# Kernel tuning notes

Hardware: AMD Instinct MI355X
Metric: run time of the kernel (lower is better)

The kernel has to match this reference:

```python
import jax, jax.numpy as jnp
import numpy as np

B, T, H, NH, HD = 2, 2048, 2048, 16, 128


def setup_inputs() -> dict:
    key = jax.random.key(0)
    k1, k2, k3 = jax.random.split(key, 3)
    hidden_states = jax.random.normal(k1, (B, T, H), dtype=jnp.float32)
    w_qkv = jax.random.normal(k2, (3 * H, H), dtype=jnp.float32) * (1.0 / np.sqrt(H))
    w_out = jax.random.normal(k3, (H, H), dtype=jnp.float32) * (1.0 / np.sqrt(H))
    return {"hidden_states": hidden_states, "w_qkv": w_qkv, "w_out": w_out}


def reference(hidden_states, w_qkv, w_out):
    scale = 1.0 / np.sqrt(HD)
    # qkv projection: torch Linear is x @ W.T with W [out, in]
    qkv = jnp.einsum('bth,oh->bto', hidden_states, w_qkv)  # [B, T, 3H]
    q, k, v = jnp.split(qkv, 3, axis=2)
    # [B, NH, T, HD]
    q = q.reshape(B, T, NH, HD).transpose(0, 2, 1, 3)
    k = k.reshape(B, T, NH, HD).transpose(0, 2, 1, 3)
    v = v.reshape(B, T, NH, HD).transpose(0, 2, 1, 3)
    scores = jnp.einsum('bhqd,bhkd->bhqk', q, k) * scale  # [B, NH, T, T]
    mask = jnp.tril(jnp.ones((T, T), dtype=bool))  # causal
    scores = jnp.where(mask[None, None], scores, -jnp.inf)
    probs = jax.nn.softmax(scores, axis=-1)
    attn = jnp.einsum('bhqk,bhkd->bhqd', probs, v)  # [B, NH, T, HD]
    attn = attn.transpose(0, 2, 1, 3).reshape(B, T, H)
    out = jnp.einsum('bth,oh->bto', attn, w_out)
    return out
```

## Files before the change

kernel.cpp:

```cpp
#include <hip/hip_runtime.h>
#include <cstdint>
#include <cstddef>

typedef _Float16 f16x8 __attribute__((ext_vector_type(8)));
typedef _Float16 f16x4 __attribute__((ext_vector_type(4)));
typedef float    f32x4 __attribute__((ext_vector_type(4)));
typedef unsigned short ushort_t;

#define LOG2E 1.4426950408889634f

constexpr int BATCH = 2;
constexpr int TSEQ  = 2048;
constexpr int HID   = 2048;
constexpr int NH    = 16;
constexpr int HD    = 128;
constexpr int GK    = 2048;
constexpr int NKT   = GK / 64;

__device__ inline f32x4 mfma16(f16x8 a, f16x8 b, f32x4 c) {
    return __builtin_amdgcn_mfma_f32_16x16x32_f16(a, b, c, 0, 0, 0);
}

__device__ inline void async_copy16(const void* src, void* dst_lds) {
    __builtin_amdgcn_global_load_lds(
        (const __attribute__((address_space(1))) uint32_t*)src,
        (__attribute__((address_space(3))) uint32_t*)dst_lds, 16, 0, 0);
}

__global__ __launch_bounds__(256)
void cast_f32_f16(const float4* __restrict__ in, f16x4* __restrict__ out, int n4) {
    int i = blockIdx.x * 256 + threadIdx.x;
    if (i >= n4) return;
    float4 v = in[i];
    f16x4 o = { (_Float16)v.x, (_Float16)v.y, (_Float16)v.z, (_Float16)v.w };
    out[i] = o;
}

template <int MODE>
__global__ __launch_bounds__(512, 2)
void gemm_bt(const _Float16* __restrict__ A, const _Float16* __restrict__ B,
             float* __restrict__ C, _Float16* __restrict__ Qo,
             _Float16* __restrict__ Ko, _Float16* __restrict__ Vo, int NB) {
    __shared__ __align__(16) _Float16 As[3][256 * 64];
    __shared__ __align__(16) _Float16 Bs[3][128 * 64];

    const int tid  = threadIdx.x;
    const int lane = tid & 63;
    const int w    = tid >> 6;
    const int l15  = lane & 15;
    const int lq   = lane >> 4;
    const int wr   = w >> 1, wc = w & 1;

    const int bid = (int)blockIdx.x;
    const int cpx = (int)gridDim.x >> 3;
    const int swz = (bid & 7) * cpx + (bid >> 3);
    const int bn  = swz % NB, bm = swz / NB;
    const int m0  = bm * 256, n0 = bn * 128;

    const _Float16* Ab = A + (size_t)m0 * GK;
    const _Float16* Bb = B + (size_t)n0 * GK;

    auto stage = [&](int t, int b) {
        const int k0 = t * 64;
        #pragma unroll
        for (int it = 0; it < 4; ++it) {
            const int slot = it * 512 + tid;
            const int row = slot >> 3, c16 = slot & 7;
            const int srcb = c16 ^ (row & 7);
            async_copy16(Ab + (size_t)row * GK + k0 + srcb * 8,
                         (char*)As[b] + slot * 16);
        }
        #pragma unroll
        for (int it = 0; it < 2; ++it) {
            const int slot = it * 512 + tid;
            const int row = slot >> 3, c16 = slot & 7;
            const int srcb = c16 ^ (row & 7);
            async_copy16(Bb + (size_t)row * GK + k0 + srcb * 8,
                         (char*)Bs[b] + slot * 16);
        }
    };

    f32x4 acc[4][4] = {};

    stage(0, 0);
    stage(1, 1);

    for (int t = 0; t < NKT; ++t) {
        if (t + 1 < NKT) asm volatile("s_waitcnt vmcnt(6)" ::: "memory");
        else             asm volatile("s_waitcnt vmcnt(0)" ::: "memory");
        __builtin_amdgcn_s_barrier();
        __builtin_amdgcn_sched_barrier(0);

        const char* At_ = (const char*)As[t % 3];
        const char* Bt_ = (const char*)Bs[t % 3];

        f16x8 af[4][2], bff[4][2];
        #pragma unroll
        for (int i = 0; i < 4; ++i)
            #pragma unroll
            for (int kk = 0; kk < 2; ++kk) {
                const int ra = wr * 64 + i * 16 + l15;
                af[i][kk]  = *(const f16x8*)(At_ + ra * 128 + (((kk * 4 + lq) ^ (ra & 7)) << 4));
                const int rb = wc * 64 + i * 16 + l15;
                bff[i][kk] = *(const f16x8*)(Bt_ + rb * 128 + (((kk * 4 + lq) ^ (rb & 7)) << 4));
            }

        if (t + 2 < NKT) stage(t + 2, (t + 2) % 3);

        __builtin_amdgcn_s_setprio(1);
        #pragma unroll
        for (int kk = 0; kk < 2; ++kk)
            #pragma unroll
            for (int i = 0; i < 4; ++i)
                #pragma unroll
                for (int j = 0; j < 4; ++j)
                    acc[i][j] = mfma16(af[i][kk], bff[j][kk], acc[i][j]);
        __builtin_amdgcn_s_setprio(0);
    }

    if (MODE == 0) {
        #pragma unroll
        for (int j = 0; j < 4; ++j) {
            const int ncol = n0 + wc * 64 + j * 16 + l15;
            const int which = ncol >> 11;
            const int oo = ncol & 2047;
            const int head = oo >> 7;
            const int d = oo & 127;
            _Float16* dst = (which == 0) ? Qo : (which == 1) ? Ko : Vo;
            const float scl = (which == 0) ? 0.08838834764831845f : 1.0f;
            #pragma unroll
            for (int i = 0; i < 4; ++i) {
                #pragma unroll
                for (int r = 0; r < 4; ++r) {
                    const int m = m0 + wr * 64 + i * 16 + lq * 4 + r;
                    const int b = m >> 11, tt = m & 2047;
                    dst[((size_t)(b * NH + head) * TSEQ + tt) * HD + d] =
                        (_Float16)(acc[i][j][r] * scl);
                }
            }
        }
    } else {
        #pragma unroll
        for (int i = 0; i < 4; ++i)
            #pragma unroll
            for (int j = 0; j < 4; ++j)
                #pragma unroll
                for (int r = 0; r < 4; ++r) {
                    const int m = m0 + wr * 64 + i * 16 + lq * 4 + r;
                    const int n = n0 + wc * 64 + j * 16 + l15;
                    C[(size_t)m * HID + n] = acc[i][j][r];
                }
    }
}

__global__ __launch_bounds__(512)
void attn_fwd(const _Float16* __restrict__ Q, const _Float16* __restrict__ K,
              const _Float16* __restrict__ V, _Float16* __restrict__ O) {
    __shared__ __align__(16) char Ks[2][64 * 256];
    __shared__ __align__(16) char Vt[2][128 * 128];
    __shared__ __align__(16) char Ps[8][2048];

    const int tid  = threadIdx.x;
    const int lane = tid & 63;
    const int w    = tid >> 6;
    const int l15  = lane & 15;
    const int lq   = lane >> 4;

    const int qt = 15 - ((int)blockIdx.x >> 5);
    const int bh = (int)blockIdx.x & 31;
    const int b = bh >> 4, h = bh & 15;

    const size_t base = (size_t)bh * TSEQ * HD;
    const _Float16* Qp = Q + base;
    const _Float16* Kp = K + base;
    const _Float16* Vp = V + base;

    const int q0 = qt * 128;
    const int NT = 2 * qt + 2;

    const int qrow = q0 + w * 16 + l15;
    f16x8 qf[4];
    #pragma unroll
    for (int ks = 0; ks < 4; ++ks)
        qf[ks] = *(const f16x8*)(Qp + (size_t)qrow * HD + ks * 32 + lq * 8);

    f32x4 o[8] = {};
    float m_run[4], l_run[4];
    #pragma unroll
    for (int r = 0; r < 4; ++r) { m_run[r] = -1e30f; l_run[r] = 0.0f; }

    char* Pb = Ps[w];
    uint4 vv[2];

    auto loadV = [&](int t) {
        const int kv0 = t * 64;
        #pragma unroll
        for (int it = 0; it < 2; ++it) {
            const int slot = it * 512 + tid;
            const int row = slot >> 4, c8 = slot & 15;
            vv[it] = *(const uint4*)(Vp + (size_t)(kv0 + row) * HD + c8 * 8);
        }
    };
    auto stageK = [&](int t, int buf) {
        const int kv0 = t * 64;
        #pragma unroll
        for (int it = 0; it < 2; ++it) {
            const int slot = it * 512 + tid;
            const int row = slot >> 4, c16 = slot & 15;
            const int srcb = c16 ^ (row & 7);
            async_copy16(Kp + (size_t)(kv0 + row) * HD + srcb * 8, Ks[buf] + slot * 16);
        }
    };
    auto writeV = [&](int buf) {
        #pragma unroll
        for (int it = 0; it < 2; ++it) {
            const int slot = it * 512 + tid;
            const int row = slot >> 4, c8 = slot & 15;
            const uint32_t wrd[4] = {vv[it].x, vv[it].y, vv[it].z, vv[it].w};
            #pragma unroll
            for (int p2 = 0; p2 < 4; ++p2) {
                const int d0 = c8 * 8 + p2 * 2, d1 = d0 + 1;
                int b0 = d0 * 128 + row * 2; b0 ^= (d0 & 7) << 4;
                int b1 = d1 * 128 + row * 2; b1 ^= (d1 & 7) << 4;
                *(ushort_t*)(Vt[buf] + b0) = (ushort_t)(wrd[p2] & 0xffffu);
                *(ushort_t*)(Vt[buf] + b1) = (ushort_t)(wrd[p2] >> 16);
            }
        }
    };

    loadV(0);
    stageK(0, 0);

    int cur = 0;
    for (int t = 0; t < NT; ++t) {
        writeV(cur);
        __syncthreads();
        if (t + 1 < NT) {
            loadV(t + 1);
            stageK(t + 1, cur ^ 1);
        }

        const int kv0 = t * 64;
        const bool skipw = (kv0 > q0 + w * 16 + 15);
        if (!skipw) {
            f32x4 s[4] = {};
            #pragma unroll
            for (int ks = 0; ks < 4; ++ks) {
                #pragma unroll
                for (int nf = 0; nf < 4; ++nf) {
                    const int r   = nf * 16 + l15;
                    const int blk = (ks * 4 + lq) ^ (r & 7);
                    const f16x8 kf = *(const f16x8*)(Ks[cur] + r * 256 + blk * 16);
                    s[nf] = mfma16(qf[ks], kf, s[nf]);
                }
            }

            if (kv0 + 63 > q0 + w * 16) {
                #pragma unroll
                for (int nf = 0; nf < 4; ++nf) {
                    const int kvp = kv0 + nf * 16 + l15;
                    #pragma unroll
                    for (int r = 0; r < 4; ++r)
                        if (kvp > q0 + w * 16 + lq * 4 + r) s[nf][r] = -1e30f;
                }
            }

            float alpha[4];
            #pragma unroll
            for (int r = 0; r < 4; ++r) {
                float v = fmaxf(fmaxf(s[0][r], s[1][r]), fmaxf(s[2][r], s[3][r]));
                v = fmaxf(v, __shfl_xor(v, 1));
                v = fmaxf(v, __shfl_xor(v, 2));
                v = fmaxf(v, __shfl_xor(v, 4));
                v = fmaxf(v, __shfl_xor(v, 8));
                const float mn = fmaxf(m_run[r], v);
                alpha[r] = __builtin_exp2f((m_run[r] - mn) * LOG2E);
                m_run[r] = mn;
            }

            float ps[4] = {0.f, 0.f, 0.f, 0.f};
            #pragma unroll
            for (int nf = 0; nf < 4; ++nf) {
                #pragma unroll
                for (int r = 0; r < 4; ++r) {
                    const float p = __builtin_exp2f((s[nf][r] - m_run[r]) * LOG2E);
                    ps[r] += p;
                    const int qp = lq * 4 + r;
                    int byt = qp * 128 + (nf * 16 + l15) * 2;
                    byt ^= (qp & 7) << 4;
                    union { _Float16 hf; ushort_t u; } cv;
                    cv.hf = (_Float16)p;
                    *(ushort_t*)(Pb + byt) = cv.u;
                }
            }
            #pragma unroll
            for (int r = 0; r < 4; ++r) {
                float v = ps[r];
                v += __shfl_xor(v, 1);
                v += __shfl_xor(v, 2);
                v += __shfl_xor(v, 4);
                v += __shfl_xor(v, 8);
                l_run[r] = l_run[r] * alpha[r] + v;
            }
            #pragma unroll
            for (int df = 0; df < 8; ++df)
                #pragma unroll
                for (int r = 0; r < 4; ++r)
                    o[df][r] *= alpha[r];

            #pragma unroll
            for (int ks2 = 0; ks2 < 2; ++ks2) {
                const int pblk = (ks2 * 4 + lq) ^ (l15 & 7);
                const f16x8 pf = *(const f16x8*)(Pb + l15 * 128 + pblk * 16);
                #pragma unroll
                for (int df = 0; df < 8; ++df) {
                    const int vr   = df * 16 + l15;
                    const int vblk = (ks2 * 4 + lq) ^ (vr & 7);
                    const f16x8 vf = *(const f16x8*)(Vt[cur] + vr * 128 + vblk * 16);
                    o[df] = mfma16(pf, vf, o[df]);
                }
            }
        }
        cur ^= 1;
    }

    #pragma unroll
    for (int r = 0; r < 4; ++r) l_run[r] = 1.0f / l_run[r];
    #pragma unroll
    for (int df = 0; df < 8; ++df) {
        #pragma unroll
        for (int r = 0; r < 4; ++r) {
            const int qg = q0 + w * 16 + lq * 4 + r;
            const int dg = df * 16 + l15;
            O[((size_t)(b * TSEQ + qg)) * HID + h * HD + dg] = (_Float16)(o[df][r] * l_run[r]);
        }
    }
}

extern "C" void kernel_launch(void* const* d_in, const int* in_sizes, int n_in,
                              void* d_out, int out_size, void* d_ws, size_t ws_size,
                              hipStream_t stream) {
    (void)in_sizes; (void)n_in; (void)out_size; (void)ws_size;
    const float* hs   = (const float*)d_in[0];
    const float* wqkv = (const float*)d_in[1];
    const float* wout = (const float*)d_in[2];

    char* ws = (char*)d_ws;
    size_t off = 0;
    _Float16* hs_h   = (_Float16*)(ws + off); off += (size_t)BATCH * TSEQ * HID * 2;
    _Float16* wqkv_h = (_Float16*)(ws + off); off += (size_t)3 * HID * HID * 2;
    _Float16* wout_h = (_Float16*)(ws + off); off += (size_t)HID * HID * 2;
    _Float16* Qh     = (_Float16*)(ws + off); off += (size_t)BATCH * NH * TSEQ * HD * 2;
    _Float16* Kh     = (_Float16*)(ws + off); off += (size_t)BATCH * NH * TSEQ * HD * 2;
    _Float16* Vh     = (_Float16*)(ws + off); off += (size_t)BATCH * NH * TSEQ * HD * 2;
    _Float16* At     = (_Float16*)(ws + off); off += (size_t)BATCH * TSEQ * HID * 2;

    const int n4_hs   = BATCH * TSEQ * HID / 4;
    const int n4_wqkv = 3 * HID * HID / 4;
    const int n4_wout = HID * HID / 4;
    cast_f32_f16<<<dim3((n4_hs   + 255) / 256), dim3(256), 0, stream>>>((const float4*)hs,   (f16x4*)hs_h,   n4_hs);
    cast_f32_f16<<<dim3((n4_wqkv + 255) / 256), dim3(256), 0, stream>>>((const float4*)wqkv, (f16x4*)wqkv_h, n4_wqkv);
    cast_f32_f16<<<dim3((n4_wout + 255) / 256), dim3(256), 0, stream>>>((const float4*)wout, (f16x4*)wout_h, n4_wout);

    gemm_bt<0><<<dim3(768), dim3(512), 0, stream>>>(
        hs_h, wqkv_h, nullptr, Qh, Kh, Vh, 48);

    attn_fwd<<<dim3(512), dim3(512), 0, stream>>>(Qh, Kh, Vh, At);

    gemm_bt<1><<<dim3(256), dim3(512), 0, stream>>>(
        At, wout_h, (float*)d_out, nullptr, nullptr, nullptr, 16);
}
```

Measured before the change: 323.2 us.

## Pair causal query tiles per block, add lazy rescale and MFMA priority

Each attention block now handles two query tiles (qt and 15-qt) one after the other, so every block does the same amount of causal work and the grid shrinks to 256 blocks, one per CU. Online softmax rescaling of o and l is skipped unless some row's max grows by more than a threshold. MFMA sections are wrapped in s_setprio, and V global loads are remapped so each wave reads a column chunk across 64 rows. The per-wave skip of fully masked tiles is removed, so waves whose rows lie entirely before the tile now compute masked rows. Lazy rescaling lets exponents run up to about 2^7 above the stored max, which carries some fp16 overflow risk for P.

```diff
diff --git a/kernel.cpp b/kernel.cpp
--- a/kernel.cpp
+++ b/kernel.cpp
@@ -166,8 +166,8 @@
     const int l15  = lane & 15;
     const int lq   = lane >> 4;
 
-    const int qt = 15 - ((int)blockIdx.x >> 5);
-    const int bh = (int)blockIdx.x & 31;
+    const int bh   = (int)blockIdx.x & 31;
+    const int pair = (int)blockIdx.x >> 5;
     const int b = bh >> 4, h = bh & 15;
 
     const size_t base = (size_t)bh * TSEQ * HD;
@@ -175,75 +175,74 @@
     const _Float16* Kp = K + base;
     const _Float16* Vp = V + base;
 
-    const int q0 = qt * 128;
-    const int NT = 2 * qt + 2;
-
-    const int qrow = q0 + w * 16 + l15;
-    f16x8 qf[4];
-    #pragma unroll
-    for (int ks = 0; ks < 4; ++ks)
-        qf[ks] = *(const f16x8*)(Qp + (size_t)qrow * HD + ks * 32 + lq * 8);
-
-    f32x4 o[8] = {};
-    float m_run[4], l_run[4];
-    #pragma unroll
-    for (int r = 0; r < 4; ++r) { m_run[r] = -1e30f; l_run[r] = 0.0f; }
-
-    char* Pb = Ps[w];
     uint4 vv[2];
-
     auto loadV = [&](int t) {
-        const int kv0 = t * 64;
         #pragma unroll
         for (int it = 0; it < 2; ++it) {
-            const int slot = it * 512 + tid;
-            const int row = slot >> 4, c8 = slot & 15;
-            vv[it] = *(const uint4*)(Vp + (size_t)(kv0 + row) * HD + c8 * 8);
+            const int c8 = it * 8 + w;
+            vv[it] = *(const uint4*)(Vp + (size_t)(t * 64 + lane) * HD + c8 * 8);
         }
     };
     auto stageK = [&](int t, int buf) {
-        const int kv0 = t * 64;
         #pragma unroll
         for (int it = 0; it < 2; ++it) {
             const int slot = it * 512 + tid;
             const int row = slot >> 4, c16 = slot & 15;
             const int srcb = c16 ^ (row & 7);
-            async_copy16(Kp + (size_t)(kv0 + row) * HD + srcb * 8, Ks[buf] + slot * 16);
+            async_copy16(Kp + (size_t)(t * 64 + row) * HD + srcb * 8, Ks[buf] + slot * 16);
         }
     };
     auto writeV = [&](int buf) {
         #pragma unroll
         for (int it = 0; it < 2; ++it) {
-            const int slot = it * 512 + tid;
-            const int row = slot >> 4, c8 = slot & 15;
+            const int c8 = it * 8 + w;
             const uint32_t wrd[4] = {vv[it].x, vv[it].y, vv[it].z, vv[it].w};
             #pragma unroll
             for (int p2 = 0; p2 < 4; ++p2) {
                 const int d0 = c8 * 8 + p2 * 2, d1 = d0 + 1;
-                int b0 = d0 * 128 + row * 2; b0 ^= (d0 & 7) << 4;
-                int b1 = d1 * 128 + row * 2; b1 ^= (d1 & 7) << 4;
+                int b0 = d0 * 128 + lane * 2; b0 ^= (d0 & 7) << 4;
+                int b1 = d1 * 128 + lane * 2; b1 ^= (d1 & 7) << 4;
                 *(ushort_t*)(Vt[buf] + b0) = (ushort_t)(wrd[p2] & 0xffffu);
                 *(ushort_t*)(Vt[buf] + b1) = (ushort_t)(wrd[p2] >> 16);
             }
         }
     };
 
-    loadV(0);
-    stageK(0, 0);
-
-    int cur = 0;
-    for (int t = 0; t < NT; ++t) {
-        writeV(cur);
-        __syncthreads();
-        if (t + 1 < NT) {
-            loadV(t + 1);
-            stageK(t + 1, cur ^ 1);
-        }
-
-        const int kv0 = t * 64;
-        const bool skipw = (kv0 > q0 + w * 16 + 15);
-        if (!skipw) {
+    char* Pb = Ps[w];
+
+    for (int phase = 0; phase < 2; ++phase) {
+        const int qt = phase ? pair : (15 - pair);
+        const int q0 = qt * 128;
+        const int NT = 2 * qt + 2;
+
+        if (phase) __syncthreads();
+
+        const int qrow = q0 + w * 16 + l15;
+        f16x8 qf[4];
+        #pragma unroll
+        for (int ks = 0; ks < 4; ++ks)
+            qf[ks] = *(const f16x8*)(Qp + (size_t)qrow * HD + ks * 32 + lq * 8);
+
+        f32x4 o[8] = {};
+        float m_run[4], l_run[4];
+        #pragma unroll
+        for (int r = 0; r < 4; ++r) { m_run[r] = -1e30f; l_run[r] = 0.0f; }
+
+        loadV(0);
+        stageK(0, 0);
+
+        int cur = 0;
+        for (int t = 0; t < NT; ++t) {
+            writeV(cur);
+            __syncthreads();
+            if (t + 1 < NT) {
+                loadV(t + 1);
+                stageK(t + 1, cur ^ 1);
+            }
+
+            const int kv0 = t * 64;
             f32x4 s[4] = {};
+            __builtin_amdgcn_s_setprio(1);
             #pragma unroll
             for (int ks = 0; ks < 4; ++ks) {
                 #pragma unroll
@@ -254,6 +253,7 @@
                     s[nf] = mfma16(qf[ks], kf, s[nf]);
                 }
             }
+            __builtin_amdgcn_s_setprio(0);
 
             if (kv0 + 63 > q0 + w * 16) {
                 #pragma unroll
@@ -265,7 +265,8 @@
                 }
             }
 
-            float alpha[4];
+            float tmax[4];
+            bool need = false;
             #pragma unroll
             for (int r = 0; r < 4; ++r) {
                 float v = fmaxf(fmaxf(s[0][r], s[1][r]), fmaxf(s[2][r], s[3][r]));
@@ -273,9 +274,23 @@
                 v = fmaxf(v, __shfl_xor(v, 2));
                 v = fmaxf(v, __shfl_xor(v, 4));
                 v = fmaxf(v, __shfl_xor(v, 8));
-                const float mn = fmaxf(m_run[r], v);
-                alpha[r] = __builtin_exp2f((m_run[r] - mn) * LOG2E);
-                m_run[r] = mn;
+                tmax[r] = v;
+                need = need || (v > m_run[r] + 5.0f);
+            }
+            if (__any(need)) {
+                float alpha[4];
+                #pragma unroll
+                for (int r = 0; r < 4; ++r) {
+                    const float mn = fmaxf(m_run[r], tmax[r]);
+                    alpha[r] = __builtin_exp2f((m_run[r] - mn) * LOG2E);
+                    m_run[r] = mn;
+                    l_run[r] *= alpha[r];
+                }
+                #pragma unroll
+                for (int df = 0; df < 8; ++df)
+                    #pragma unroll
+                    for (int r = 0; r < 4; ++r)
+                        o[df][r] *= alpha[r];
             }
 
             float ps[4] = {0.f, 0.f, 0.f, 0.f};
@@ -300,14 +315,10 @@
                 v += __shfl_xor(v, 2);
                 v += __shfl_xor(v, 4);
                 v += __shfl_xor(v, 8);
-                l_run[r] = l_run[r] * alpha[r] + v;
-            }
-            #pragma unroll
-            for (int df = 0; df < 8; ++df)
-                #pragma unroll
-                for (int r = 0; r < 4; ++r)
-                    o[df][r] *= alpha[r];
-
+                l_run[r] += v;
+            }
+
+            __builtin_amdgcn_s_setprio(1);
             #pragma unroll
             for (int ks2 = 0; ks2 < 2; ++ks2) {
                 const int pblk = (ks2 * 4 + lq) ^ (l15 & 7);
@@ -320,19 +331,21 @@
                     o[df] = mfma16(pf, vf, o[df]);
                 }
             }
-        }
-        cur ^= 1;
-    }
-
-    #pragma unroll
-    for (int r = 0; r < 4; ++r) l_run[r] = 1.0f / l_run[r];
-    #pragma unroll
-    for (int df = 0; df < 8; ++df) {
-        #pragma unroll
-        for (int r = 0; r < 4; ++r) {
-            const int qg = q0 + w * 16 + lq * 4 + r;
-            const int dg = df * 16 + l15;
-            O[((size_t)(b * TSEQ + qg)) * HID + h * HD + dg] = (_Float16)(o[df][r] * l_run[r]);
+            __builtin_amdgcn_s_setprio(0);
+            cur ^= 1;
+        }
+
+        #pragma unroll
+        for (int r = 0; r < 4; ++r) l_run[r] = 1.0f / l_run[r];
+        #pragma unroll
+        for (int df = 0; df < 8; ++df) {
+            #pragma unroll
+            for (int r = 0; r < 4; ++r) {
+                const int qg = q0 + w * 16 + lq * 4 + r;
+                const int dg = df * 16 + l15;
+                O[((size_t)(b * TSEQ + qg)) * HID + h * HD + dg] =
+                    (_Float16)(o[df][r] * l_run[r]);
+            }
         }
     }
 }
@@ -365,7 +378,7 @@
     gemm_bt<0><<<dim3(768), dim3(512), 0, stream>>>(
         hs_h, wqkv_h, nullptr, Qh, Kh, Vh, 48);
 
-    attn_fwd<<<dim3(512), dim3(512), 0, stream>>>(Qh, Kh, Vh, At);
+    attn_fwd<<<dim3(256), dim3(512), 0, stream>>>(Qh, Kh, Vh, At);
 
     gemm_bt<1><<<dim3(256), dim3(512), 0, stream>>>(
         At, wout_h, (float*)d_out, nullptr, nullptr, nullptr, 16);
```

After: 294.1 us. -9.0%, faster.
